# Kernel tuning notes

Measured on AMD Instinct MI355X. Metric: run time of the kernel, lower is better.

## Reference

```python
import jax, jax.numpy as jnp
import numpy as np

HEADS = 8
DIM_HEAD = 128
LN_EPS = 1e-5


def setup_inputs() -> dict:
    key = jax.random.key(0)
    ks = jax.random.split(key, 4)
    N, M, C, V, T = 64, 2, 64, 15, 256
    dim = C * V              # 960
    inner = HEADS * DIM_HEAD # 1024
    return {
        "x": jax.random.normal(ks[0], (N, M, C, V, T), dtype=jnp.float32),
        "ln_g": jnp.ones((dim,), jnp.float32),
        "ln_b": jnp.zeros((dim,), jnp.float32),
        "w_qkv": jax.random.normal(ks[1], (dim, 3 * inner), dtype=jnp.float32) * (dim ** -0.5),
        "w_out": jax.random.normal(ks[2], (inner, dim), dtype=jnp.float32) * (inner ** -0.5),
        "b_out": jnp.zeros((dim,), jnp.float32),
        "w_lin": jax.random.normal(ks[3], (T, T), dtype=jnp.float32) * (T ** -0.5),
        "b_lin": jnp.zeros((T,), jnp.float32),
    }


def reference(x, ln_g, ln_b, w_qkv, w_out, b_out, w_lin, b_lin):
    N, M, C, V, T = x.shape
    dim = C * V
    # [N, M, C, V, T] -> [N*M, T, C*V]
    xs = jnp.transpose(x, (0, 1, 4, 2, 3)).reshape(N * M, T, dim)

    # PreNorm (LayerNorm over last dim)
    mu = jnp.mean(xs, axis=-1, keepdims=True)
    var = jnp.mean(jnp.square(xs - mu), axis=-1, keepdims=True)
    xn = (xs - mu) * jax.lax.rsqrt(var + LN_EPS) * ln_g + ln_b

    # Attention
    qkv = xn @ w_qkv  # [NM, T, 3*inner]
    q, k, v = jnp.split(qkv, 3, axis=-1)
    def to_heads(t):
        return jnp.transpose(t.reshape(N * M, T, HEADS, DIM_HEAD), (0, 2, 1, 3))
    q, k, v = to_heads(q), to_heads(k), to_heads(v)  # [NM, H, T, D]
    scale = DIM_HEAD ** -0.5
    dots = jnp.einsum('nhid,nhjd->nhij', q, k) * scale
    attn = jax.nn.softmax(dots, axis=-1)
    out = jnp.einsum('nhij,nhjd->nhid', attn, v)
    out = jnp.transpose(out, (0, 2, 1, 3)).reshape(N * M, T, HEADS * DIM_HEAD)
    out = out @ w_out + b_out

    # Residual
    xs = out + xs

    # back to [N, M, C, V, T], then Linear over T + tanh
    x2 = jnp.transpose(xs.reshape(N, M, T, C, V), (0, 1, 3, 4, 2))
    y = jnp.tanh(x2 @ w_lin.T + b_lin)
    return y
```

## Files before the change

kernel.cpp:

```cpp
#include <hip/hip_runtime.h>

typedef unsigned short ushort;
using short8 = __attribute__((ext_vector_type(8))) short;
using f32x4  = __attribute__((ext_vector_type(4))) float;
using i32x4  = __attribute__((ext_vector_type(4))) int;
using us4    = __attribute__((ext_vector_type(4))) ushort;

static __device__ __forceinline__ float bf2f(ushort u) {
  union { unsigned int i; float f; } x; x.i = ((unsigned int)u) << 16; return x.f;
}
static __device__ __forceinline__ ushort f2bf(float f) {
  union { float f; unsigned int i; } x; x.f = f;
  unsigned int u = x.i;
  unsigned int r = u + 0x7fffu + ((u >> 16) & 1u);
  return (ushort)(r >> 16);
}

#define GLOAD16(gp, lp)                                                   \
  __builtin_amdgcn_global_load_lds(                                      \
      (const __attribute__((address_space(1))) void*)(gp),               \
      (__attribute__((address_space(3))) void*)(lp), 16, 0, 0)

__global__ __launch_bounds__(256) void wtrans_kernel(const float* __restrict__ in,
                                                     ushort* __restrict__ out,
                                                     int R, int C) {
  __shared__ float sl[32][33];
  int tx = threadIdx.x & 31, ty = threadIdx.x >> 5;
  int c0 = blockIdx.x * 32, r0 = blockIdx.y * 32;
#pragma unroll
  for (int s = 0; s < 4; s++) {
    int r = r0 + ty + s * 8;
    int c = c0 + tx;
    sl[ty + s * 8][tx] = (c < C) ? in[(size_t)r * C + c] : 0.f;
  }
  __syncthreads();
#pragma unroll
  for (int s = 0; s < 4; s++) {
    int c = c0 + ty + s * 8;
    int r = r0 + tx;
    out[(size_t)c * R + r] = f2bf(sl[tx][ty + s * 8]);
  }
}

__global__ void wsplit_kernel(const float* __restrict__ in, ushort* __restrict__ hi,
                              ushort* __restrict__ lo, int n) {
  int i = blockIdx.x * 256 + threadIdx.x;
  if (i < n) {
    float v = in[i];
    ushort h = f2bf(v);
    hi[i] = h;
    lo[i] = f2bf(v - bf2f(h));
  }
}

__global__ __launch_bounds__(256) void ln_fused_kernel(const float* __restrict__ x,
                                                       const float* __restrict__ g,
                                                       const float* __restrict__ b,
                                                       ushort* __restrict__ xn) {
  __shared__ float sl[960][20];
  __shared__ float smean[16], srstd[16];
  int tid = threadIdx.x;
  int nm = blockIdx.y;
  int t0 = blockIdx.x * 16;

  int r0 = tid >> 2, c4 = (tid & 3) * 4;
#pragma unroll
  for (int it = 0; it < 15; it++) {
    int r = it * 64 + r0;
    float4 v = *(const float4*)&x[((size_t)nm * 960 + r) * 256 + t0 + c4];
    *(float4*)&sl[r][c4] = v;
  }
  __syncthreads();

  int tg = tid >> 4, lt = tid & 15;
  float s = 0.f, ss = 0.f;
#pragma unroll 4
  for (int k = 0; k < 60; k++) {
    float v = sl[lt + k * 16][tg];
    s += v; ss += v * v;
  }
#pragma unroll
  for (int d = 1; d < 16; d <<= 1) {
    s += __shfl_xor(s, d, 64);
    ss += __shfl_xor(ss, d, 64);
  }
  if (lt == 0) {
    float mean = s * (1.f / 960.f);
    float var = ss * (1.f / 960.f) - mean * mean;
    smean[tg] = mean;
    srstd[tg] = rsqrtf(var + 1e-5f);
  }
  __syncthreads();

  float gg[4], bb[4];
#pragma unroll
  for (int c = 0; c < 4; c++) {
    int col = c * 256 + tid;
    if (col < 960) { gg[c] = g[col]; bb[c] = b[col]; }
  }
#pragma unroll
  for (int t = 0; t < 16; t++) {
    float mean = smean[t], rstd = srstd[t];
#pragma unroll
    for (int c = 0; c < 4; c++) {
      int col = c * 256 + tid;
      if (col < 960)
        xn[((size_t)nm * 256 + t0 + t) * 960 + col] =
            f2bf((sl[col][t] - mean) * rstd * gg[c] + bb[c]);
    }
  }
}

template <int MODE>
__global__ __launch_bounds__(512, 2) void gemm256(
    const ushort* __restrict__ A, int lda, const ushort* __restrict__ BT, int ldb, int nkt,
    const ushort* __restrict__ Alo, const ushort* __restrict__ Blo,
    ushort* __restrict__ o0, ushort* __restrict__ o1, ushort* __restrict__ o2,
    const float* __restrict__ bias, float* __restrict__ fout) {
  __shared__ char smem[131072];
  int tid = threadIdx.x;
  int l = tid & 63, w = tid >> 6;
  int wr = w >> 2, wc = w & 3;
  int lr = l & 15, lg = l >> 4;
  int cb = blockIdx.x * 256, rb = blockIdx.y * 256;

  int srow = tid >> 2;
  int scol = ((tid & 3) ^ ((tid >> 3) & 3)) * 8;

  int swz = (lg ^ ((lr >> 1) & 3)) << 4;
  const char* ArdB = smem + (wr * 128 + lr) * 64 + swz;
  const char* BrdB = smem + 65536 + (wc * 64 + lr) * 64 + swz;

  auto stage_half = [&](int kt, int kk, int isB) {
    const ushort* P; int ld; int k0;
    if (MODE == 2) {
      int seg = kt >> 2; k0 = (kt & 3) * 64 + kk * 32;
      P = isB ? ((seg == 1) ? Blo : BT) : ((seg == 2) ? Alo : A);
      ld = 256;
    } else {
      P = isB ? BT : A; ld = isB ? ldb : lda; k0 = kt * 64 + kk * 32;
    }
    const ushort* gp = P + (size_t)((isB ? cb : rb) + srow) * ld + k0 + scol;
    char* dst = smem + isB * 65536 + (kt & 1) * 32768 + kk * 16384 + tid * 16;
    GLOAD16(gp, dst);
    GLOAD16(gp + (size_t)128 * ld, dst + 8192);
  };

  f32x4 acc[8][4];
#pragma unroll
  for (int i = 0; i < 8; i++)
#pragma unroll
    for (int j = 0; j < 4; j++) acc[i][j] = (f32x4){0.f, 0.f, 0.f, 0.f};

  stage_half(0, 0, 0); stage_half(0, 0, 1); stage_half(0, 1, 0); stage_half(0, 1, 1);
  asm volatile("s_waitcnt vmcnt(4)" ::: "memory");
  __builtin_amdgcn_s_barrier();

  for (int t = 0; t < nkt; t++) {
    const char* Ard = ArdB + (t & 1) * 32768;
    const char* Brd = BrdB + (t & 1) * 32768;
    bool st = (t + 1 < nkt);
    short8 a[4], b[4];

#pragma unroll
    for (int j = 0; j < 4; j++) b[j] = *(const short8*)(Brd + j * 1024);
#pragma unroll
    for (int i = 0; i < 4; i++) a[i] = *(const short8*)(Ard + i * 1024);
    if (st) stage_half(t + 1, 0, 0);
    __builtin_amdgcn_s_barrier();
    __builtin_amdgcn_s_setprio(1);
#pragma unroll
    for (int i = 0; i < 4; i++)
#pragma unroll
      for (int j = 0; j < 4; j++)
        acc[i][j] = __builtin_amdgcn_mfma_f32_16x16x32_bf16(a[i], b[j], acc[i][j], 0, 0, 0);
    __builtin_amdgcn_s_setprio(0);
    __builtin_amdgcn_s_barrier();

#pragma unroll
    for (int i = 0; i < 4; i++) a[i] = *(const short8*)(Ard + (4 + i) * 1024);
    if (st) stage_half(t + 1, 0, 1);
    __builtin_amdgcn_s_barrier();
    __builtin_amdgcn_s_setprio(1);
#pragma unroll
    for (int i = 0; i < 4; i++)
#pragma unroll
      for (int j = 0; j < 4; j++)
        acc[4 + i][j] = __builtin_amdgcn_mfma_f32_16x16x32_bf16(a[i], b[j], acc[4 + i][j], 0, 0, 0);
    __builtin_amdgcn_s_setprio(0);
    if (st) asm volatile("s_waitcnt vmcnt(4)" ::: "memory");
    else    asm volatile("s_waitcnt vmcnt(0)" ::: "memory");
    __builtin_amdgcn_s_barrier();

#pragma unroll
    for (int j = 0; j < 4; j++) b[j] = *(const short8*)(Brd + 16384 + j * 1024);
#pragma unroll
    for (int i = 0; i < 4; i++) a[i] = *(const short8*)(Ard + 16384 + i * 1024);
    if (st) stage_half(t + 1, 1, 0);
    __builtin_amdgcn_s_barrier();
    __builtin_amdgcn_s_setprio(1);
#pragma unroll
    for (int i = 0; i < 4; i++)
#pragma unroll
      for (int j = 0; j < 4; j++)
        acc[i][j] = __builtin_amdgcn_mfma_f32_16x16x32_bf16(a[i], b[j], acc[i][j], 0, 0, 0);
    __builtin_amdgcn_s_setprio(0);
    __builtin_amdgcn_s_barrier();

#pragma unroll
    for (int i = 0; i < 4; i++) a[i] = *(const short8*)(Ard + 16384 + (4 + i) * 1024);
    if (st) stage_half(t + 1, 1, 1);
    __builtin_amdgcn_s_barrier();
    __builtin_amdgcn_s_setprio(1);
#pragma unroll
    for (int i = 0; i < 4; i++)
#pragma unroll
      for (int j = 0; j < 4; j++)
        acc[4 + i][j] = __builtin_amdgcn_mfma_f32_16x16x32_bf16(a[i], b[j], acc[4 + i][j], 0, 0, 0);
    __builtin_amdgcn_s_setprio(0);
    if (st) asm volatile("s_waitcnt vmcnt(4)" ::: "memory");
    else    asm volatile("s_waitcnt vmcnt(0)" ::: "memory");
    __builtin_amdgcn_s_barrier();
  }

  int row0 = rb + wr * 128, col0 = cb + wc * 64;
  if (MODE == 0) {
    int nm = rb >> 8;
    int which = cb >> 10;
#pragma unroll
    for (int i = 0; i < 8; i++)
#pragma unroll
      for (int j = 0; j < 4; j++) {
        f32x4 v = acc[i][j];
        int col = col0 + j * 16 + lr;
        int cl = col & 1023;
        int h = cl >> 7, d = cl & 127;
        int nmh = nm * 8 + h;
        int t0 = wr * 128 + i * 16 + lg * 4;
        if (which == 2) {
          us4 pk;
          pk.x = f2bf(v[0]); pk.y = f2bf(v[1]); pk.z = f2bf(v[2]); pk.w = f2bf(v[3]);
          *(us4*)&o2[((size_t)nmh * 128 + d) * 256 + t0] = pk;
        } else if (which == 0) {
#pragma unroll
          for (int r = 0; r < 4; r++)
            o0[((size_t)nmh * 256 + t0 + r) * 128 + d] = f2bf(v[r] * 0.08838834764831845f);
        } else {
#pragma unroll
          for (int r = 0; r < 4; r++)
            o1[((size_t)nmh * 256 + t0 + r) * 128 + d] = f2bf(v[r]);
        }
      }
  } else if (MODE == 1) {
    int nm = rb >> 8;
#pragma unroll
    for (int i = 0; i < 8; i++)
#pragma unroll
      for (int j = 0; j < 4; j++) {
        f32x4 v = acc[i][j];
        int col = col0 + j * 16 + lr;
        float bb = (col < 960) ? bias[col] : 0.f;
        int t0 = wr * 128 + i * 16 + lg * 4;
        us4 pk;
        pk.x = f2bf(v[0] + bb); pk.y = f2bf(v[1] + bb);
        pk.z = f2bf(v[2] + bb); pk.w = f2bf(v[3] + bb);
        *(us4*)&o0[((size_t)nm * 1024 + col) * 256 + t0] = pk;
      }
  } else {
#pragma unroll
    for (int i = 0; i < 8; i++)
#pragma unroll
      for (int j = 0; j < 4; j++) {
        f32x4 v = acc[i][j];
        int col = col0 + j * 16 + lr;
        float bb = bias[col];
#pragma unroll
        for (int r = 0; r < 4; r++) {
          int row = row0 + i * 16 + lg * 4 + r;
          fout[(size_t)row * 256 + col] = tanhf(v[r] + bb);
        }
      }
  }
}

__global__ __launch_bounds__(512, 2) void attn2_kernel(const ushort* __restrict__ q,
                                                       const ushort* __restrict__ kb,
                                                       const ushort* __restrict__ vT,
                                                       ushort* __restrict__ ao) {
  __shared__ char smem[131072];
  int tid = threadIdx.x;
  int l = tid & 63, w = tid >> 6;
  int lr = l & 15, lg = l >> 4;
  int nmh = blockIdx.x;

  const ushort* kbase = kb + (size_t)nmh * 32768;
  const ushort* vbase = vT + (size_t)nmh * 32768;

#pragma unroll
  for (int u = 0; u < 8; u++) {
    int row = u * 32 + w * 4 + (l >> 4);
    int slot = l & 15;
    GLOAD16(kbase + row * 128 + ((slot ^ (row & 7)) * 8), smem + u * 8192 + w * 1024);
  }
  short8 aq[2][4];
  {
    const ushort* qp = q + (size_t)nmh * 32768 + (size_t)(w * 32 + lr) * 128 + lg * 8;
#pragma unroll
    for (int i = 0; i < 2; i++)
#pragma unroll
      for (int kk = 0; kk < 4; kk++) aq[i][kk] = *(const short8*)(qp + i * 2048 + kk * 32);
  }
#pragma unroll
  for (int u = 0; u < 8; u++) {
    int row = u * 16 + w * 2 + (l >> 5);
    int slot = l & 31;
    GLOAD16(vbase + row * 256 + ((slot ^ (row & 7)) * 8),
            smem + 65536 + u * 8192 + w * 1024);
  }
  asm volatile("s_waitcnt vmcnt(8)" ::: "memory");
  __builtin_amdgcn_s_barrier();

  f32x4 s_acc[2][16];
#pragma unroll
  for (int i = 0; i < 2; i++)
#pragma unroll
    for (int j = 0; j < 16; j++) s_acc[i][j] = (f32x4){0.f, 0.f, 0.f, 0.f};
#pragma unroll
  for (int j = 0; j < 16; j++) {
    short8 bk[4];
#pragma unroll
    for (int kk = 0; kk < 4; kk++)
      bk[kk] = *(const short8*)(smem + (j * 16 + lr) * 256 + (((kk * 4 + lg) ^ (lr & 7)) << 4));
#pragma unroll
    for (int i = 0; i < 2; i++)
#pragma unroll
      for (int kk = 0; kk < 4; kk++)
        s_acc[i][j] = __builtin_amdgcn_mfma_f32_16x16x32_bf16(aq[i][kk], bk[kk], s_acc[i][j], 0, 0, 0);
  }

  float m[2][4], sum[2][4], rs[2][4];
#pragma unroll
  for (int i = 0; i < 2; i++)
#pragma unroll
    for (int r = 0; r < 4; r++) m[i][r] = -1e30f;
#pragma unroll
  for (int i = 0; i < 2; i++)
#pragma unroll
    for (int j = 0; j < 16; j++)
#pragma unroll
      for (int r = 0; r < 4; r++) m[i][r] = fmaxf(m[i][r], s_acc[i][j][r]);
#pragma unroll
  for (int d = 1; d < 16; d <<= 1)
#pragma unroll
    for (int i = 0; i < 2; i++)
#pragma unroll
      for (int r = 0; r < 4; r++) m[i][r] = fmaxf(m[i][r], __shfl_xor(m[i][r], d, 64));
#pragma unroll
  for (int i = 0; i < 2; i++)
#pragma unroll
    for (int r = 0; r < 4; r++) sum[i][r] = 0.f;
#pragma unroll
  for (int i = 0; i < 2; i++)
#pragma unroll
    for (int j = 0; j < 16; j++)
#pragma unroll
      for (int r = 0; r < 4; r++) {
        float p = __expf(s_acc[i][j][r] - m[i][r]);
        s_acc[i][j][r] = p;
        sum[i][r] += p;
      }
#pragma unroll
  for (int d = 1; d < 16; d <<= 1)
#pragma unroll
    for (int i = 0; i < 2; i++)
#pragma unroll
      for (int r = 0; r < 4; r++) sum[i][r] += __shfl_xor(sum[i][r], d, 64);
#pragma unroll
  for (int i = 0; i < 2; i++)
#pragma unroll
    for (int r = 0; r < 4; r++) rs[i][r] = 1.f / sum[i][r];

  __builtin_amdgcn_s_barrier();
  asm volatile("s_waitcnt vmcnt(0)" ::: "memory");

  char* Pb = smem + w * 4608;
  f32x4 o_acc[2][8];
#pragma unroll
  for (int i = 0; i < 2; i++)
#pragma unroll
    for (int j = 0; j < 8; j++) o_acc[i][j] = (f32x4){0.f, 0.f, 0.f, 0.f};

#pragma unroll
  for (int ct = 0; ct < 4; ct++) {
#pragma unroll
    for (int i = 0; i < 2; i++)
#pragma unroll
      for (int jj = 0; jj < 4; jj++)
#pragma unroll
        for (int r = 0; r < 4; r++)
          *(ushort*)(Pb + (i * 16 + lg * 4 + r) * 144 + (jj * 16 + lr) * 2) =
              f2bf(s_acc[i][ct * 4 + jj][r]);
    short8 pa[2][2];
#pragma unroll
    for (int i = 0; i < 2; i++)
#pragma unroll
      for (int kk = 0; kk < 2; kk++)
        pa[i][kk] = *(const short8*)(Pb + (i * 16 + lr) * 144 + kk * 64 + lg * 16);
#pragma unroll
    for (int j = 0; j < 8; j++) {
      short8 bv[2];
#pragma unroll
      for (int kk = 0; kk < 2; kk++)
        bv[kk] = *(const short8*)(smem + 65536 + (j * 16 + lr) * 512 +
                                  (((ct * 8 + kk * 4 + lg) ^ (lr & 7)) << 4));
#pragma unroll
      for (int i = 0; i < 2; i++)
#pragma unroll
        for (int kk = 0; kk < 2; kk++)
          o_acc[i][j] = __builtin_amdgcn_mfma_f32_16x16x32_bf16(pa[i][kk], bv[kk], o_acc[i][j], 0, 0, 0);
    }
  }

  int nm = nmh >> 3, h = nmh & 7;
#pragma unroll
  for (int i = 0; i < 2; i++)
#pragma unroll
    for (int j = 0; j < 8; j++)
#pragma unroll
      for (int r = 0; r < 4; r++) {
        int t = w * 32 + i * 16 + lg * 4 + r;
        int d = h * 128 + j * 16 + lr;
        ao[((size_t)nm * 256 + t) * 1024 + d] = f2bf(o_acc[i][j][r] * rs[i][r]);
      }
}

__global__ __launch_bounds__(256) void x2split_kernel(const float* __restrict__ x,
                                                      const ushort* __restrict__ projT,
                                                      ushort* __restrict__ hi,
                                                      ushort* __restrict__ lo) {
  int nm = blockIdx.y;
  int cv = blockIdx.x * 4 + (threadIdx.x >> 6);
  int t = (threadIdx.x & 63) * 4;
  size_t xi = ((size_t)nm * 960 + cv) * 256 + t;
  f32x4 xv = *(const f32x4*)&x[xi];
  us4 pv = *(const us4*)&projT[((size_t)nm * 1024 + cv) * 256 + t];
  us4 h, lo4;
#pragma unroll
  for (int e = 0; e < 4; e++) {
    float s = xv[e] + bf2f(pv[e]);
    ushort hh = f2bf(s);
    h[e] = hh;
    lo4[e] = f2bf(s - bf2f(hh));
  }
  *(us4*)&hi[xi] = h;
  *(us4*)&lo[xi] = lo4;
}

extern "C" void kernel_launch(void* const* d_in, const int* in_sizes, int n_in,
                              void* d_out, int out_size, void* d_ws, size_t ws_size,
                              hipStream_t stream) {
  const float* x = (const float*)d_in[0];
  const float* ln_g = (const float*)d_in[1];
  const float* ln_b = (const float*)d_in[2];
  const float* w_qkv = (const float*)d_in[3];
  const float* w_out = (const float*)d_in[4];
  const float* b_out = (const float*)d_in[5];
  const float* w_lin = (const float*)d_in[6];
  const float* b_lin = (const float*)d_in[7];
  float* out = (float*)d_out;

  char* ws = (char*)d_ws;
  size_t off = 0;
  auto alloc = [&](size_t bytes) -> void* {
    void* p = ws + off;
    off = (off + bytes + 255) & ~(size_t)255;
    return p;
  };

  ushort* wqkvT = (ushort*)alloc((size_t)3072 * 960 * 2);
  ushort* woutT = (ushort*)alloc((size_t)1024 * 1024 * 2);
  ushort* whi   = (ushort*)alloc((size_t)65536 * 2);
  ushort* wlo   = (ushort*)alloc((size_t)65536 * 2);
  ushort* xn    = (ushort*)alloc((size_t)32768 * 960 * 2);
  ushort* qbuf  = (ushort*)alloc((size_t)1024 * 256 * 128 * 2);
  ushort* kbuf  = (ushort*)alloc((size_t)1024 * 256 * 128 * 2);
  ushort* vTbuf = (ushort*)alloc((size_t)1024 * 256 * 128 * 2);
  ushort* attnout = (ushort*)alloc((size_t)32768 * 1024 * 2);
  ushort* projT = qbuf;
  ushort* x2hi  = kbuf;
  ushort* x2lo  = vTbuf;

  wtrans_kernel<<<dim3(96, 30), 256, 0, stream>>>(w_qkv, wqkvT, 960, 3072);
  wtrans_kernel<<<dim3(32, 32), 256, 0, stream>>>(w_out, woutT, 1024, 960);
  wsplit_kernel<<<dim3(256), 256, 0, stream>>>(w_lin, whi, wlo, 65536);

  ln_fused_kernel<<<dim3(16, 128), 256, 0, stream>>>(x, ln_g, ln_b, xn);

  gemm256<0><<<dim3(12, 128), 512, 0, stream>>>(xn, 960, wqkvT, 960, 15, nullptr, nullptr,
                                                qbuf, kbuf, vTbuf, nullptr, nullptr);
  attn2_kernel<<<dim3(1024), 512, 0, stream>>>(qbuf, kbuf, vTbuf, attnout);
  gemm256<1><<<dim3(4, 128), 512, 0, stream>>>(attnout, 1024, woutT, 1024, 16, nullptr, nullptr,
                                               projT, nullptr, nullptr, b_out, nullptr);
  x2split_kernel<<<dim3(240, 128), 256, 0, stream>>>(x, projT, x2hi, x2lo);
  gemm256<2><<<dim3(1, 480), 512, 0, stream>>>(x2hi, 256, whi, 256, 12, x2lo, wlo,
                                               nullptr, nullptr, nullptr, b_lin, out);
}
```

Measured before the change: 622.8 us.

## Switch GEMM to 32x32x16 MFMA and fuse residual hi/lo split into out-proj epilogue

Replaces the 16x16x32 bf16 MFMA tiles in the shared GEMM with 32x32x16 instructions, using fewer, larger accumulators and a new LDS read pattern. This aims to raise MFMA throughput per LDS byte read. It also folds the residual add and the bf16 hi/lo split into the MODE 1 epilogue, which removes the separate x2split kernel and the projT intermediate round trip through memory. The risks are the changed register pressure and a new LDS bank-conflict pattern.

```diff
diff --git a/kernel.cpp b/kernel.cpp
--- a/kernel.cpp
+++ b/kernel.cpp
@@ -3,6 +3,7 @@
 typedef unsigned short ushort;
 using short8 = __attribute__((ext_vector_type(8))) short;
 using f32x4  = __attribute__((ext_vector_type(4))) float;
+using f32x16 = __attribute__((ext_vector_type(16))) float;
 using i32x4  = __attribute__((ext_vector_type(4))) int;
 using us4    = __attribute__((ext_vector_type(4))) ushort;
 
@@ -116,20 +117,23 @@
     const ushort* __restrict__ A, int lda, const ushort* __restrict__ BT, int ldb, int nkt,
     const ushort* __restrict__ Alo, const ushort* __restrict__ Blo,
     ushort* __restrict__ o0, ushort* __restrict__ o1, ushort* __restrict__ o2,
-    const float* __restrict__ bias, float* __restrict__ fout) {
+    const float* __restrict__ bias, const float* __restrict__ xres,
+    float* __restrict__ fout) {
   __shared__ char smem[131072];
   int tid = threadIdx.x;
   int l = tid & 63, w = tid >> 6;
   int wr = w >> 2, wc = w & 3;
-  int lr = l & 15, lg = l >> 4;
+  int l31 = l & 31, hi = l >> 5;
   int cb = blockIdx.x * 256, rb = blockIdx.y * 256;
 
   int srow = tid >> 2;
   int scol = ((tid & 3) ^ ((tid >> 3) & 3)) * 8;
 
-  int swz = (lg ^ ((lr >> 1) & 3)) << 4;
-  const char* ArdB = smem + (wr * 128 + lr) * 64 + swz;
-  const char* BrdB = smem + 65536 + (wc * 64 + lr) * 64 + swz;
+  int phs = (l31 >> 1) & 3;
+  int so0 = ((0 + hi) ^ phs) << 4;
+  int so1 = ((2 + hi) ^ phs) << 4;
+  const char* Abase0 = smem + (wr * 128 + l31) * 64;
+  const char* Bbase0 = smem + 65536 + (wc * 64 + l31) * 64;
 
   auto stage_half = [&](int kt, int kk, int isB) {
     const ushort* P; int ld; int k0;
@@ -146,139 +150,190 @@
     GLOAD16(gp + (size_t)128 * ld, dst + 8192);
   };
 
-  f32x4 acc[8][4];
-#pragma unroll
-  for (int i = 0; i < 8; i++)
-#pragma unroll
-    for (int j = 0; j < 4; j++) acc[i][j] = (f32x4){0.f, 0.f, 0.f, 0.f};
+  f32x16 acc[4][2];
+#pragma unroll
+  for (int i = 0; i < 4; i++)
+#pragma unroll
+    for (int j = 0; j < 2; j++)
+#pragma unroll
+      for (int e = 0; e < 16; e++) acc[i][j][e] = 0.f;
 
   stage_half(0, 0, 0); stage_half(0, 0, 1); stage_half(0, 1, 0); stage_half(0, 1, 1);
   asm volatile("s_waitcnt vmcnt(4)" ::: "memory");
   __builtin_amdgcn_s_barrier();
 
   for (int t = 0; t < nkt; t++) {
-    const char* Ard = ArdB + (t & 1) * 32768;
-    const char* Brd = BrdB + (t & 1) * 32768;
+    const char* Ab = Abase0 + (t & 1) * 32768;
+    const char* Bb = Bbase0 + (t & 1) * 32768;
     bool st = (t + 1 < nkt);
-    short8 a[4], b[4];
-
-#pragma unroll
-    for (int j = 0; j < 4; j++) b[j] = *(const short8*)(Brd + j * 1024);
-#pragma unroll
-    for (int i = 0; i < 4; i++) a[i] = *(const short8*)(Ard + i * 1024);
+    short8 a[2][2], b[2][2];
+
+#pragma unroll
+    for (int nj = 0; nj < 2; nj++) {
+      b[nj][0] = *(const short8*)(Bb + nj * 2048 + so0);
+      b[nj][1] = *(const short8*)(Bb + nj * 2048 + so1);
+    }
+#pragma unroll
+    for (int mi = 0; mi < 2; mi++) {
+      a[mi][0] = *(const short8*)(Ab + mi * 2048 + so0);
+      a[mi][1] = *(const short8*)(Ab + mi * 2048 + so1);
+    }
     if (st) stage_half(t + 1, 0, 0);
     __builtin_amdgcn_s_barrier();
     __builtin_amdgcn_s_setprio(1);
 #pragma unroll
-    for (int i = 0; i < 4; i++)
-#pragma unroll
-      for (int j = 0; j < 4; j++)
-        acc[i][j] = __builtin_amdgcn_mfma_f32_16x16x32_bf16(a[i], b[j], acc[i][j], 0, 0, 0);
+    for (int mi = 0; mi < 2; mi++)
+#pragma unroll
+      for (int nj = 0; nj < 2; nj++)
+#pragma unroll
+        for (int s = 0; s < 2; s++)
+          acc[mi][nj] = __builtin_amdgcn_mfma_f32_32x32x16_bf16(a[mi][s], b[nj][s], acc[mi][nj], 0, 0, 0);
     __builtin_amdgcn_s_setprio(0);
     __builtin_amdgcn_s_barrier();
 
 #pragma unroll
-    for (int i = 0; i < 4; i++) a[i] = *(const short8*)(Ard + (4 + i) * 1024);
+    for (int mi = 0; mi < 2; mi++) {
+      a[mi][0] = *(const short8*)(Ab + (2 + mi) * 2048 + so0);
+      a[mi][1] = *(const short8*)(Ab + (2 + mi) * 2048 + so1);
+    }
     if (st) stage_half(t + 1, 0, 1);
     __builtin_amdgcn_s_barrier();
     __builtin_amdgcn_s_setprio(1);
 #pragma unroll
-    for (int i = 0; i < 4; i++)
-#pragma unroll
-      for (int j = 0; j < 4; j++)
-        acc[4 + i][j] = __builtin_amdgcn_mfma_f32_16x16x32_bf16(a[i], b[j], acc[4 + i][j], 0, 0, 0);
+    for (int mi = 0; mi < 2; mi++)
+#pragma unroll
+      for (int nj = 0; nj < 2; nj++)
+#pragma unroll
+        for (int s = 0; s < 2; s++)
+          acc[2 + mi][nj] = __builtin_amdgcn_mfma_f32_32x32x16_bf16(a[mi][s], b[nj][s], acc[2 + mi][nj], 0, 0, 0);
     __builtin_amdgcn_s_setprio(0);
     if (st) asm volatile("s_waitcnt vmcnt(4)" ::: "memory");
     else    asm volatile("s_waitcnt vmcnt(0)" ::: "memory");
     __builtin_amdgcn_s_barrier();
 
 #pragma unroll
-    for (int j = 0; j < 4; j++) b[j] = *(const short8*)(Brd + 16384 + j * 1024);
-#pragma unroll
-    for (int i = 0; i < 4; i++) a[i] = *(const short8*)(Ard + 16384 + i * 1024);
+    for (int nj = 0; nj < 2; nj++) {
+      b[nj][0] = *(const short8*)(Bb + 16384 + nj * 2048 + so0);
+      b[nj][1] = *(const short8*)(Bb + 16384 + nj * 2048 + so1);
+    }
+#pragma unroll
+    for (int mi = 0; mi < 2; mi++) {
+      a[mi][0] = *(const short8*)(Ab + 16384 + mi * 2048 + so0);
+      a[mi][1] = *(const short8*)(Ab + 16384 + mi * 2048 + so1);
+    }
     if (st) stage_half(t + 1, 1, 0);
     __builtin_amdgcn_s_barrier();
     __builtin_amdgcn_s_setprio(1);
 #pragma unroll
-    for (int i = 0; i < 4; i++)
-#pragma unroll
-      for (int j = 0; j < 4; j++)
-        acc[i][j] = __builtin_amdgcn_mfma_f32_16x16x32_bf16(a[i], b[j], acc[i][j], 0, 0, 0);
+    for (int mi = 0; mi < 2; mi++)
+#pragma unroll
+      for (int nj = 0; nj < 2; nj++)
+#pragma unroll
+        for (int s = 0; s < 2; s++)
+          acc[mi][nj] = __builtin_amdgcn_mfma_f32_32x32x16_bf16(a[mi][s], b[nj][s], acc[mi][nj], 0, 0, 0);
     __builtin_amdgcn_s_setprio(0);
     __builtin_amdgcn_s_barrier();
 
 #pragma unroll
-    for (int i = 0; i < 4; i++) a[i] = *(const short8*)(Ard + 16384 + (4 + i) * 1024);
+    for (int mi = 0; mi < 2; mi++) {
+      a[mi][0] = *(const short8*)(Ab + 16384 + (2 + mi) * 2048 + so0);
+      a[mi][1] = *(const short8*)(Ab + 16384 + (2 + mi) * 2048 + so1);
+    }
     if (st) stage_half(t + 1, 1, 1);
     __builtin_amdgcn_s_barrier();
     __builtin_amdgcn_s_setprio(1);
 #pragma unroll
-    for (int i = 0; i < 4; i++)
-#pragma unroll
-      for (int j = 0; j < 4; j++)
-        acc[4 + i][j] = __builtin_amdgcn_mfma_f32_16x16x32_bf16(a[i], b[j], acc[4 + i][j], 0, 0, 0);
+    for (int mi = 0; mi < 2; mi++)
+#pragma unroll
+      for (int nj = 0; nj < 2; nj++)
+#pragma unroll
+        for (int s = 0; s < 2; s++)
+          acc[2 + mi][nj] = __builtin_amdgcn_mfma_f32_32x32x16_bf16(a[mi][s], b[nj][s], acc[2 + mi][nj], 0, 0, 0);
     __builtin_amdgcn_s_setprio(0);
     if (st) asm volatile("s_waitcnt vmcnt(4)" ::: "memory");
     else    asm volatile("s_waitcnt vmcnt(0)" ::: "memory");
     __builtin_amdgcn_s_barrier();
   }
 
-  int row0 = rb + wr * 128, col0 = cb + wc * 64;
   if (MODE == 0) {
     int nm = rb >> 8;
     int which = cb >> 10;
 #pragma unroll
-    for (int i = 0; i < 8; i++)
-#pragma unroll
-      for (int j = 0; j < 4; j++) {
-        f32x4 v = acc[i][j];
-        int col = col0 + j * 16 + lr;
+    for (int mi = 0; mi < 4; mi++)
+#pragma unroll
+      for (int nj = 0; nj < 2; nj++) {
+        f32x16 v = acc[mi][nj];
+        int col = cb + wc * 64 + nj * 32 + l31;
         int cl = col & 1023;
         int h = cl >> 7, d = cl & 127;
         int nmh = nm * 8 + h;
-        int t0 = wr * 128 + i * 16 + lg * 4;
+        int tb = wr * 128 + mi * 32 + 4 * hi;
         if (which == 2) {
-          us4 pk;
-          pk.x = f2bf(v[0]); pk.y = f2bf(v[1]); pk.z = f2bf(v[2]); pk.w = f2bf(v[3]);
-          *(us4*)&o2[((size_t)nmh * 128 + d) * 256 + t0] = pk;
+#pragma unroll
+          for (int q = 0; q < 4; q++) {
+            us4 pk;
+            pk.x = f2bf(v[4 * q]);     pk.y = f2bf(v[4 * q + 1]);
+            pk.z = f2bf(v[4 * q + 2]); pk.w = f2bf(v[4 * q + 3]);
+            *(us4*)&o2[((size_t)nmh * 128 + d) * 256 + tb + 8 * q] = pk;
+          }
         } else if (which == 0) {
 #pragma unroll
-          for (int r = 0; r < 4; r++)
-            o0[((size_t)nmh * 256 + t0 + r) * 128 + d] = f2bf(v[r] * 0.08838834764831845f);
+          for (int q = 0; q < 4; q++)
+#pragma unroll
+            for (int r = 0; r < 4; r++)
+              o0[((size_t)nmh * 256 + tb + 8 * q + r) * 128 + d] =
+                  f2bf(v[4 * q + r] * 0.08838834764831845f);
         } else {
 #pragma unroll
-          for (int r = 0; r < 4; r++)
-            o1[((size_t)nmh * 256 + t0 + r) * 128 + d] = f2bf(v[r]);
+          for (int q = 0; q < 4; q++)
+#pragma unroll
+            for (int r = 0; r < 4; r++)
+              o1[((size_t)nmh * 256 + tb + 8 * q + r) * 128 + d] = f2bf(v[4 * q + r]);
         }
       }
   } else if (MODE == 1) {
     int nm = rb >> 8;
 #pragma unroll
-    for (int i = 0; i < 8; i++)
-#pragma unroll
-      for (int j = 0; j < 4; j++) {
-        f32x4 v = acc[i][j];
-        int col = col0 + j * 16 + lr;
-        float bb = (col < 960) ? bias[col] : 0.f;
-        int t0 = wr * 128 + i * 16 + lg * 4;
-        us4 pk;
-        pk.x = f2bf(v[0] + bb); pk.y = f2bf(v[1] + bb);
-        pk.z = f2bf(v[2] + bb); pk.w = f2bf(v[3] + bb);
-        *(us4*)&o0[((size_t)nm * 1024 + col) * 256 + t0] = pk;
+    for (int mi = 0; mi < 4; mi++)
+#pragma unroll
+      for (int nj = 0; nj < 2; nj++) {
+        int col = cb + wc * 64 + nj * 32 + l31;
+        if (col < 960) {
+          f32x16 v = acc[mi][nj];
+          float bb = bias[col];
+          size_t rowb = ((size_t)nm * 960 + col) * 256;
+          int tb = wr * 128 + mi * 32 + 4 * hi;
+#pragma unroll
+          for (int q = 0; q < 4; q++) {
+            int t0 = tb + 8 * q;
+            f32x4 xv = *(const f32x4*)&xres[rowb + t0];
+            us4 h4, l4;
+#pragma unroll
+            for (int e = 0; e < 4; e++) {
+              float s = xv[e] + v[4 * q + e] + bb;
+              ushort hh = f2bf(s);
+              h4[e] = hh;
+              l4[e] = f2bf(s - bf2f(hh));
+            }
+            *(us4*)&o0[rowb + t0] = h4;
+            *(us4*)&o1[rowb + t0] = l4;
+          }
+        }
       }
   } else {
 #pragma unroll
-    for (int i = 0; i < 8; i++)
-#pragma unroll
-      for (int j = 0; j < 4; j++) {
-        f32x4 v = acc[i][j];
-        int col = col0 + j * 16 + lr;
+    for (int mi = 0; mi < 4; mi++)
+#pragma unroll
+      for (int nj = 0; nj < 2; nj++) {
+        f32x16 v = acc[mi][nj];
+        int col = cb + wc * 64 + nj * 32 + l31;
         float bb = bias[col];
-#pragma unroll
-        for (int r = 0; r < 4; r++) {
-          int row = row0 + i * 16 + lg * 4 + r;
-          fout[(size_t)row * 256 + col] = tanhf(v[r] + bb);
-        }
+        int rbase = rb + wr * 128 + mi * 32 + 4 * hi;
+#pragma unroll
+        for (int q = 0; q < 4; q++)
+#pragma unroll
+          for (int r = 0; r < 4; r++)
+            fout[(size_t)(rbase + 8 * q + r) * 256 + col] = tanhf(v[4 * q + r] + bb);
       }
   }
 }
@@ -432,28 +487,6 @@
         int d = h * 128 + j * 16 + lr;
         ao[((size_t)nm * 256 + t) * 1024 + d] = f2bf(o_acc[i][j][r] * rs[i][r]);
       }
-}
-
-__global__ __launch_bounds__(256) void x2split_kernel(const float* __restrict__ x,
-                                                      const ushort* __restrict__ projT,
-                                                      ushort* __restrict__ hi,
-                                                      ushort* __restrict__ lo) {
-  int nm = blockIdx.y;
-  int cv = blockIdx.x * 4 + (threadIdx.x >> 6);
-  int t = (threadIdx.x & 63) * 4;
-  size_t xi = ((size_t)nm * 960 + cv) * 256 + t;
-  f32x4 xv = *(const f32x4*)&x[xi];
-  us4 pv = *(const us4*)&projT[((size_t)nm * 1024 + cv) * 256 + t];
-  us4 h, lo4;
-#pragma unroll
-  for (int e = 0; e < 4; e++) {
-    float s = xv[e] + bf2f(pv[e]);
-    ushort hh = f2bf(s);
-    h[e] = hh;
-    lo4[e] = f2bf(s - bf2f(hh));
-  }
-  *(us4*)&hi[xi] = h;
-  *(us4*)&lo[xi] = lo4;
 }
 
 extern "C" void kernel_launch(void* const* d_in, const int* in_sizes, int n_in,
@@ -486,9 +519,8 @@
   ushort* kbuf  = (ushort*)alloc((size_t)1024 * 256 * 128 * 2);
   ushort* vTbuf = (ushort*)alloc((size_t)1024 * 256 * 128 * 2);
   ushort* attnout = (ushort*)alloc((size_t)32768 * 1024 * 2);
-  ushort* projT = qbuf;
-  ushort* x2hi  = kbuf;
-  ushort* x2lo  = vTbuf;
+  ushort* x2hi  = qbuf;
+  ushort* x2lo  = kbuf;
 
   wtrans_kernel<<<dim3(96, 30), 256, 0, stream>>>(w_qkv, wqkvT, 960, 3072);
   wtrans_kernel<<<dim3(32, 32), 256, 0, stream>>>(w_out, woutT, 1024, 960);
@@ -497,11 +529,10 @@
   ln_fused_kernel<<<dim3(16, 128), 256, 0, stream>>>(x, ln_g, ln_b, xn);
 
   gemm256<0><<<dim3(12, 128), 512, 0, stream>>>(xn, 960, wqkvT, 960, 15, nullptr, nullptr,
-                                                qbuf, kbuf, vTbuf, nullptr, nullptr);
+                                                qbuf, kbuf, vTbuf, nullptr, nullptr, nullptr);
   attn2_kernel<<<dim3(1024), 512, 0, stream>>>(qbuf, kbuf, vTbuf, attnout);
   gemm256<1><<<dim3(4, 128), 512, 0, stream>>>(attnout, 1024, woutT, 1024, 16, nullptr, nullptr,
-                                               projT, nullptr, nullptr, b_out, nullptr);
-  x2split_kernel<<<dim3(240, 128), 256, 0, stream>>>(x, projT, x2hi, x2lo);
+                                               x2hi, x2lo, nullptr, b_out, x, nullptr);
   gemm256<2><<<dim3(1, 480), 512, 0, stream>>>(x2hi, 256, whi, 256, 12, x2lo, wlo,
-                                               nullptr, nullptr, nullptr, b_lin, out);
-}
+                                               nullptr, nullptr, nullptr, b_lin, nullptr, out);
+}
```

Result: slower. 661.4 us (+6.2%).
